# Kernel optimization log

Measured on AMD Instinct MI355X. Metric: run time of the kernel, lower is better.

The kernel has to match this reference:

```python
import jax, jax.numpy as jnp
import numpy as np

H = 1024   # hidden_size
I = 4096   # intermediate_size
E = 8      # num_local_experts
K = 2      # num_experts_per_tok
B, S = 2, 2048


def setup_inputs() -> dict:
    key = jax.random.key(0)
    ks = jax.random.split(key, 7)
    init = lambda k, shape, fan_in: (jax.random.normal(k, shape, jnp.float32)
                                     / np.float32(np.sqrt(fan_in)))
    return {
        "x": jax.random.normal(ks[0], (B, S, H), jnp.float32),
        "router_gate": init(ks[1], (E, H), H),   # router for gate_proj
        "w_gate": init(ks[2], (E, I, H), H),     # expert weights gate_proj
        "router_up": init(ks[3], (E, H), H),     # router for up_proj
        "w_up": init(ks[4], (E, I, H), H),       # expert weights up_proj
        "router_down": init(ks[5], (E, I), I),   # router for down_proj
        "w_down": init(ks[6], (E, H, I), I),     # expert weights down_proj
    }


def _moe_linear(x, router_w, expert_w):
    """Top-K routed linear. x:[T,din] router_w:[E,din] expert_w:[E,dout,din]."""
    n_exp = router_w.shape[0]
    logits = x @ router_w.T                      # [T, E]
    vals, idx = jax.lax.top_k(logits, K)         # [T, K]
    probs = jax.nn.softmax(vals, axis=-1)        # softmax over selected experts
    onehot = jax.nn.one_hot(idx, n_exp, dtype=x.dtype)    # [T, K, E]
    combine = jnp.einsum('tk,tke->te', probs, onehot)     # [T, E] sparse combine weights
    out = jnp.zeros((x.shape[0], expert_w.shape[1]), x.dtype)
    for e in range(n_exp):  # fixed small expert count
        out = out + combine[:, e:e + 1] * (x @ expert_w[e].T)
    return out


def reference(x, router_gate, w_gate, router_up, w_up, router_down, w_down):
    b, s, h = x.shape
    xt = x.reshape(b * s, h)                     # tokens [T, H]
    g = _moe_linear(xt, router_gate, w_gate)     # [T, I]
    u = _moe_linear(xt, router_up, w_up)         # [T, I]
    inter = jax.nn.silu(g) * u                   # SwiGLU
    d = _moe_linear(inter, router_down, w_down)  # [T, H]
    return d.reshape(b, s, h)
```

## Files before the change

### kernel.cpp

```cpp
#include <hip/hip_runtime.h>
#include <cmath>

typedef float    f32x4 __attribute__((ext_vector_type(4)));
typedef _Float16 f16x8 __attribute__((ext_vector_type(8)));
typedef _Float16 f16x4 __attribute__((ext_vector_type(4)));

#define T_NUM 4096
#define H_DIM 1024
#define I_DIM 4096
#define MAXTILES 40
#define GEMMBLK 768
#define CW3BLK 4096
#define CW1BLK 4096

#define M_COUNTS   0
#define M_CURSORS  48
#define M_OFFSETS  96
#define M_NTILES   144
#define M_TILE_E   152
#define M_TILE_M   392
#define M_TOPKI    1024
#define M_TOPKP    25600
#define M_STOK     50176
#define M_SPRB     74752

__device__ __forceinline__ float wave_sum(float v) {
  v += __shfl_xor(v, 32);
  v += __shfl_xor(v, 16);
  v += __shfl_xor(v, 8);
  v += __shfl_xor(v, 4);
  v += __shfl_xor(v, 2);
  v += __shfl_xor(v, 1);
  return v;
}

__device__ __forceinline__ void topk_write(int* meta, int layer, int t, const float* v) {
  int e0 = 0; float v0 = v[0];
  #pragma unroll
  for (int e = 1; e < 8; ++e) { if (v[e] > v0) { v0 = v[e]; e0 = e; } }
  int e1 = 0; float v1 = -3.4e38f;
  #pragma unroll
  for (int e = 0; e < 8; ++e) { if (e != e0 && v[e] > v1) { v1 = v[e]; e1 = e; } }
  float ex = expf(v1 - v0);
  float p0 = 1.f / (1.f + ex);
  float p1 = ex / (1.f + ex);
  meta[M_TOPKI + (layer * T_NUM + t) * 2    ] = e0;
  meta[M_TOPKI + (layer * T_NUM + t) * 2 + 1] = e1;
  ((float*)meta)[M_TOPKP + (layer * T_NUM + t) * 2    ] = p0;
  ((float*)meta)[M_TOPKP + (layer * T_NUM + t) * 2 + 1] = p1;
}

__global__ __launch_bounds__(256) void router_gu(const float* __restrict__ x,
    const float* __restrict__ Rg, const float* __restrict__ Ru, int* __restrict__ meta)
{
  int w = threadIdx.x >> 6, lane = threadIdx.x & 63;
  int t = blockIdx.x * 4 + w;
  const float* xr = x + (size_t)t * H_DIM + lane * 4;
  f32x4 xv[4];
  #pragma unroll
  for (int c = 0; c < 4; ++c) xv[c] = *(const f32x4*)(xr + c * 256);
  float lg[8], lu[8];
  #pragma unroll
  for (int e = 0; e < 8; ++e) {
    const float* rg = Rg + (size_t)e * H_DIM + lane * 4;
    const float* ru = Ru + (size_t)e * H_DIM + lane * 4;
    float sg = 0.f, su = 0.f;
    #pragma unroll
    for (int c = 0; c < 4; ++c) {
      f32x4 a = *(const f32x4*)(rg + c * 256);
      f32x4 b = *(const f32x4*)(ru + c * 256);
      sg += a[0]*xv[c][0] + a[1]*xv[c][1] + a[2]*xv[c][2] + a[3]*xv[c][3];
      su += b[0]*xv[c][0] + b[1]*xv[c][1] + b[2]*xv[c][2] + b[3]*xv[c][3];
    }
    lg[e] = wave_sum(sg);
    lu[e] = wave_sum(su);
  }
  if (lane == 0) {
    topk_write(meta, 0, t, lg);
    topk_write(meta, 1, t, lu);
  }
}

__global__ __launch_bounds__(256) void route_finalize(int* __restrict__ meta, int l0, int nl) {
  __shared__ int cnt_s[32];
  __shared__ int off_s[32];
  __shared__ int cur_s[32];
  int tid = threadIdx.x;
  if (tid < 32) { cnt_s[tid] = 0; cur_s[tid] = 0; }
  __syncthreads();
  for (int t = tid; t < T_NUM; t += 256) {
    for (int l = l0; l < l0 + nl; ++l) {
      int li = l - l0;
      #pragma unroll
      for (int k = 0; k < 2; ++k) {
        int e = meta[M_TOPKI + (l * T_NUM + t) * 2 + k];
        atomicAdd(&cnt_s[li * 16 + k * 8 + e], 1);
      }
    }
  }
  __syncthreads();
  if (tid == 0) {
    for (int l = l0; l < l0 + nl; ++l) {
      int li = l - l0;
      int off = 0;
      for (int k = 0; k < 2; ++k) {
        int nt = 0;
        for (int e = 0; e < 8; ++e) {
          int s = (l * 2 + k) * 8 + e;
          int c = cnt_s[li * 16 + k * 8 + e];
          meta[M_COUNTS + s] = c;
          meta[M_OFFSETS + s] = off;
          off_s[li * 16 + k * 8 + e] = off;
          for (int m = 0; m < c; m += 128) {
            meta[M_TILE_E + (l * 2 + k) * MAXTILES + nt] = e;
            meta[M_TILE_M + (l * 2 + k) * MAXTILES + nt] = m;
            ++nt;
          }
          off += c;
        }
        meta[M_NTILES + l * 2 + k] = nt;
      }
    }
  }
  __syncthreads();
  for (int t = tid; t < T_NUM; t += 256) {
    for (int l = l0; l < l0 + nl; ++l) {
      int li = l - l0;
      #pragma unroll
      for (int k = 0; k < 2; ++k) {
        int e = meta[M_TOPKI + (l * T_NUM + t) * 2 + k];
        float p = ((float*)meta)[M_TOPKP + (l * T_NUM + t) * 2 + k];
        int si = li * 16 + k * 8 + e;
        int pos = off_s[si] + atomicAdd(&cur_s[si], 1);
        meta[M_STOK + l * 8192 + pos] = t;
        ((float*)meta)[M_SPRB + l * 8192 + pos] = p;
      }
    }
  }
}

template<int SPLITS, int NB, int KT>
__device__ __forceinline__ void convert_lds_body(const float* __restrict__ W,
    _Float16* __restrict__ Whi, _Float16* __restrict__ Wlo, int blk,
    _Float16* sHi, _Float16* sLo)
{
  constexpr int KTG = KT / 2;
  constexpr int K   = KT * 32;
  int panel = blk / KTG;
  int ktg   = blk - panel * KTG;
  int t = threadIdx.x;
  int r = t >> 1, h = t & 1;

  const float* src = W + ((size_t)panel * 128 + r) * K + (ktg * 2 + h) * 32;
  f32x4 v[8];
  #pragma unroll
  for (int j = 0; j < 8; ++j) v[j] = *(const f32x4*)(src + j * 4);

  #pragma unroll
  for (int fq = 0; fq < 4; ++fq) {
    f16x8 hi8, lo8;
    #pragma unroll
    for (int q = 0; q < 8; ++q) {
      int idx = fq * 8 + q;
      float x = v[idx >> 2][idx & 3];
      _Float16 hx = (_Float16)x;
      hi8[q] = hx;
      if constexpr (SPLITS == 3) lo8[q] = (_Float16)(x - (float)hx);
    }
    int loff = h * 4096 + fq * 1024 + r * 8;
    *(f16x8*)(sHi + loff) = hi8;
    if constexpr (SPLITS == 3) *(f16x8*)(sLo + loff) = lo8;
  }
  __syncthreads();

  size_t base = ((size_t)panel * KT + ktg * 2) * 4096;
  #pragma unroll
  for (int j = 0; j < 4; ++j) {
    int o = (j * 256 + t) * 8;
    *(f16x8*)(Whi + base + o) = *(const f16x8*)(sHi + o);
  }
  if constexpr (SPLITS == 3) {
    #pragma unroll
    for (int j = 0; j < 4; ++j) {
      int o = (j * 256 + t) * 8;
      *(f16x8*)(Wlo + base + o) = *(const f16x8*)(sLo + o);
    }
  }
}

__device__ __forceinline__ void gather_a_body(const float* __restrict__ X,
    _Float16* __restrict__ Apass, const int* __restrict__ meta, int layer, int kk, int gb)
{
  int pass = layer * 2 + kk;
  int tile = gb >> 5;
  int kt   = gb & 31;
  if (tile >= meta[M_NTILES + pass]) return;
  int m0   = meta[M_TILE_M + pass * MAXTILES + tile];
  int e    = meta[M_TILE_E + pass * MAXTILES + tile];
  int sidx = pass * 8 + e;
  int cnt  = meta[M_COUNTS + sidx];
  int seg  = meta[M_OFFSETS + sidx];
  const int* stok = meta + M_STOK + layer * 8192 + seg;
  size_t cb = ((size_t)tile * 32 + kt) * 8192;
  #pragma unroll
  for (int j = 0; j < 2; ++j) {
    int idx = threadIdx.x * 2 + j;
    int fq = idx >> 7, row = idx & 127;
    int m = m0 + row; if (m >= cnt) m = cnt - 1;
    const float* src = X + (size_t)stok[m] * H_DIM + kt * 32 + fq * 8;
    f32x4 v0 = *(const f32x4*)src;
    f32x4 v1 = *(const f32x4*)(src + 4);
    f16x8 h, l;
    #pragma unroll
    for (int q = 0; q < 8; ++q) {
      float v = (q < 4) ? v0[q] : v1[q - 4];
      _Float16 hv = (_Float16)v;
      h[q] = hv;
      l[q] = (_Float16)(v - (float)hv);
    }
    *(f16x8*)(Apass + cb + (size_t)idx * 8) = h;
    *(f16x8*)(Apass + cb + 4096 + (size_t)idx * 8) = l;
  }
}

__device__ __forceinline__ void gather_d_body(const _Float16* __restrict__ Gi,
    _Float16* __restrict__ Ad, const int* __restrict__ meta, int kk, int gb)
{
  int pass = 4 + kk;
  int tile = gb >> 7;
  int kt   = gb & 127;
  if (tile >= meta[M_NTILES + pass]) return;
  int m0   = meta[M_TILE_M + pass * MAXTILES + tile];
  int e    = meta[M_TILE_E + pass * MAXTILES + tile];
  int sidx = pass * 8 + e;
  int cnt  = meta[M_COUNTS + sidx];
  int seg  = meta[M_OFFSETS + sidx];
  const int* stok = meta + M_STOK + 2 * 8192 + seg;
  size_t cb = ((size_t)tile * 128 + kt) * 4096;
  #pragma unroll
  for (int j = 0; j < 2; ++j) {
    int idx = threadIdx.x * 2 + j;
    int fq = idx >> 7, row = idx & 127;
    int m = m0 + row; if (m >= cnt) m = cnt - 1;
    f16x8 h = *(const f16x8*)(Gi + (size_t)stok[m] * I_DIM + kt * 32 + fq * 8);
    *(f16x8*)(Ad + cb + (size_t)idx * 8) = h;
  }
}

__global__ __launch_bounds__(256) void fused_cw3_ga(const float* __restrict__ W,
    _Float16* __restrict__ Whi, _Float16* __restrict__ Wlo,
    const float* __restrict__ X, _Float16* __restrict__ Atgt,
    const int* __restrict__ meta, int layer, int kk)
{
  __shared__ _Float16 sHi[8192];
  __shared__ _Float16 sLo[8192];
  int b = (int)blockIdx.x;
  if (b < CW3BLK) convert_lds_body<3, 32, 32>(W, Whi, Wlo, b, sHi, sLo);
  else gather_a_body(X, Atgt, meta, layer, kk, b - CW3BLK);
}

__global__ __launch_bounds__(256) void fused_cw3x2_ga(
    const float* __restrict__ Wg, _Float16* __restrict__ Wgh, _Float16* __restrict__ Wgl,
    const float* __restrict__ Wu, _Float16* __restrict__ Wuh, _Float16* __restrict__ Wul,
    const float* __restrict__ X, _Float16* __restrict__ Atgt, const int* __restrict__ meta)
{
  __shared__ _Float16 sHi[8192];
  __shared__ _Float16 sLo[8192];
  int b = (int)blockIdx.x;
  if (b < CW3BLK) convert_lds_body<3, 32, 32>(Wg, Wgh, Wgl, b, sHi, sLo);
  else if (b < 2 * CW3BLK) convert_lds_body<3, 32, 32>(Wu, Wuh, Wul, b - CW3BLK, sHi, sLo);
  else gather_a_body(X, Atgt, meta, 0, 0, b - 2 * CW3BLK);
}

__global__ __launch_bounds__(256) void fused_cw1_gd(const float* __restrict__ W,
    _Float16* __restrict__ Whi,
    const _Float16* __restrict__ Gi, _Float16* __restrict__ Adt,
    const int* __restrict__ meta, int kk)
{
  __shared__ _Float16 sHi[8192];
  int b = (int)blockIdx.x;
  if (b < CW1BLK) convert_lds_body<1, 8, 128>(W, Whi, Whi, b, sHi, sHi);
  else gather_d_body(Gi, Adt, meta, kk, b - CW1BLK);
}

__global__ __launch_bounds__(256) void gather_a_k(const float* __restrict__ X,
    _Float16* __restrict__ Apass, const int* __restrict__ meta, int layer, int kk)
{
  gather_a_body(X, Apass, meta, layer, kk, (int)blockIdx.x);
}

__device__ __forceinline__ void gload16(const _Float16* g, _Float16* l) {
  __builtin_amdgcn_global_load_lds(
      (const __attribute__((address_space(1))) void*)g,
      (__attribute__((address_space(3))) void*)l, 16, 0, 0);
}

template<int SPLITS, int ADD, int N, int NB, int STEPS, int SPLITK, int STEAL>
__global__ __launch_bounds__(256, 3) void moe_gemm9(
    const _Float16* __restrict__ Aimg,
    const _Float16* __restrict__ Whi, const _Float16* __restrict__ Wlo,
    float* __restrict__ Out, float* __restrict__ Scr,
    const int* __restrict__ meta, int layer, int kk,
    const void* __restrict__ aux_src, _Float16* __restrict__ aux_dst,
    int alayer, int akk)
{
  constexpr int NWG = MAXTILES * NB * SPLITK;
  constexpr int Q8  = NWG / 8;
  constexpr int WCH = (SPLITS == 3) ? 1 : 2;
  constexpr int NPER = GEMMBLK / 8;

  __shared__ __align__(16) _Float16 sA[3 * 8192];

  if constexpr (STEAL == 1) {
    for (int gb = (int)blockIdx.x; gb < MAXTILES * 32; gb += GEMMBLK)
      gather_a_body((const float*)aux_src, aux_dst, meta, alayer, akk, gb);
  } else if constexpr (STEAL == 2) {
    for (int gb = (int)blockIdx.x; gb < MAXTILES * 128; gb += GEMMBLK)
      gather_d_body((const _Float16*)aux_src, aux_dst, meta, akk, gb);
  }

  int xcd  = (int)blockIdx.x & 7;
  int slot = (int)blockIdx.x >> 3;
  int pass = layer * 2 + kk;
  int ntiles = meta[M_NTILES + pass];

  int tid = threadIdx.x, lane = tid & 63, w = tid >> 6;
  int wr = w >> 1, wc = w & 1, fr = lane & 15, fq = lane >> 4;
  int aoff = (fq * 128 + wr * 64 + fr) * 8;

  for (int base = slot; base < Q8; base += NPER) {
    int logical = xcd * Q8 + base;
    int kc = 0, rem = logical;
    if constexpr (SPLITK == 2) { kc = logical / (MAXTILES * NB); rem = logical - kc * (MAXTILES * NB); }
    int tx = rem / NB;
    int ny = rem - tx * NB;
    if (tx >= ntiles) continue;

    int e    = meta[M_TILE_E + pass * MAXTILES + tx];
    int m0   = meta[M_TILE_M + pass * MAXTILES + tx];
    int sidx = pass * 8 + e;
    int cnt  = meta[M_COUNTS + sidx];
    int seg  = meta[M_OFFSETS + sidx];
    int n0   = ny * 128;

    const int*   stok = meta + M_STOK + layer * 8192 + seg;
    const float* sprb = (const float*)meta + M_SPRB + layer * 8192 + seg;

    const _Float16* At = Aimg + ((size_t)tx * SPLITK + kc) * STEPS * 8192;
    size_t wpanel = (size_t)(e * NB + ny) * (STEPS * WCH * SPLITK) * 4096;
    int kb = kc * STEPS * WCH;
    const _Float16* WhL = Whi + wpanel + (size_t)kb * 4096 + (fq * 128 + wc * 64 + fr) * 8;
    const _Float16* WlL = Wlo + wpanel + (size_t)kb * 4096 + (fq * 128 + wc * 64 + fr) * 8;

    auto stageA = [&](int it, int slot2) {
      const _Float16* s0 = At + (size_t)it * 8192 + w * 1024 + lane * 8;
      _Float16* d0 = sA + slot2 * 8192 + w * 1024;
      gload16(s0,        d0);
      gload16(s0 + 512,  d0 + 512);
      gload16(s0 + 4096, d0 + 4096);
      gload16(s0 + 4608, d0 + 4608);
    };
    auto loadW = [&](int it, f16x8 (&wh)[WCH][4], f16x8 (&wl)[1][4]) {
      #pragma unroll
      for (int c = 0; c < WCH; ++c) {
        size_t cb = (size_t)(it * WCH + c) * 4096;
        #pragma unroll
        for (int ni = 0; ni < 4; ++ni) wh[c][ni] = *(const f16x8*)(WhL + cb + ni * 128);
      }
      if constexpr (SPLITS == 3) {
        size_t cb = (size_t)it * 4096;
        #pragma unroll
        for (int ni = 0; ni < 4; ++ni) wl[0][ni] = *(const f16x8*)(WlL + cb + ni * 128);
      }
    };

    f32x4 acc[4][4];
    #pragma unroll
    for (int i = 0; i < 4; ++i)
      #pragma unroll
      for (int j = 0; j < 4; ++j) acc[i][j] = f32x4{0.f, 0.f, 0.f, 0.f};

    f16x8 w0h[WCH][4], w0l[1][4], w1h[WCH][4], w1l[1][4];
    int rc = 0, rs = 2;

    auto step = [&](int it, f16x8 (&cwh)[WCH][4], f16x8 (&cwl)[1][4],
                    f16x8 (&nwh)[WCH][4], f16x8 (&nwl)[1][4]) {
      int it2 = (it + 2 < STEPS) ? it + 2 : STEPS - 1;
      int it1 = (it + 1 < STEPS) ? it + 1 : STEPS - 1;
      stageA(it2, rs);
      loadW(it1, nwh, nwl);
      __builtin_amdgcn_sched_barrier(0);

      const _Float16* A0 = sA + rc * 8192;
      __builtin_amdgcn_s_setprio(1);
      if constexpr (SPLITS == 3) {
        f16x8 ah[4], al[4];
        #pragma unroll
        for (int mi = 0; mi < 4; ++mi) ah[mi] = *(const f16x8*)(A0 + aoff + mi * 128);
        #pragma unroll
        for (int mi = 0; mi < 4; ++mi) al[mi] = *(const f16x8*)(A0 + 4096 + aoff + mi * 128);
        #pragma unroll
        for (int mi = 0; mi < 4; ++mi)
          #pragma unroll
          for (int ni = 0; ni < 4; ++ni)
            acc[mi][ni] = __builtin_amdgcn_mfma_f32_16x16x32_f16(ah[mi], cwh[0][ni], acc[mi][ni], 0, 0, 0);
        #pragma unroll
        for (int mi = 0; mi < 4; ++mi)
          #pragma unroll
          for (int ni = 0; ni < 4; ++ni)
            acc[mi][ni] = __builtin_amdgcn_mfma_f32_16x16x32_f16(ah[mi], cwl[0][ni], acc[mi][ni], 0, 0, 0);
        #pragma unroll
        for (int mi = 0; mi < 4; ++mi)
          #pragma unroll
          for (int ni = 0; ni < 4; ++ni)
            acc[mi][ni] = __builtin_amdgcn_mfma_f32_16x16x32_f16(al[mi], cwh[0][ni], acc[mi][ni], 0, 0, 0);
      } else {
        #pragma unroll
        for (int c = 0; c < WCH; ++c) {
          f16x8 ah[4];
          #pragma unroll
          for (int mi = 0; mi < 4; ++mi) ah[mi] = *(const f16x8*)(A0 + c * 4096 + aoff + mi * 128);
          #pragma unroll
          for (int mi = 0; mi < 4; ++mi)
            #pragma unroll
            for (int ni = 0; ni < 4; ++ni)
              acc[mi][ni] = __builtin_amdgcn_mfma_f32_16x16x32_f16(ah[mi], cwh[c][ni], acc[mi][ni], 0, 0, 0);
        }
      }
      __builtin_amdgcn_s_setprio(0);

      __builtin_amdgcn_sched_barrier(0);
      asm volatile("s_waitcnt vmcnt(12)" ::: "memory");
      __builtin_amdgcn_s_barrier();
      __builtin_amdgcn_sched_barrier(0);
      rc = (rc == 2) ? 0 : rc + 1;
      rs = (rs == 2) ? 0 : rs + 1;
    };

    asm volatile("s_waitcnt vmcnt(0)" ::: "memory");
    __builtin_amdgcn_s_barrier();
    stageA(0, 0);
    stageA(1 < STEPS ? 1 : 0, 1);
    loadW(0, w0h, w0l);
    __builtin_amdgcn_sched_barrier(0);
    asm volatile("s_waitcnt vmcnt(12)" ::: "memory");
    __builtin_amdgcn_s_barrier();
    __builtin_amdgcn_sched_barrier(0);

    for (int it = 0; it < STEPS; it += 2) {
      step(it,     w0h, w0l, w1h, w1l);
      step(it + 1, w1h, w1l, w0h, w0l);
    }

    float* dst = (SPLITK == 2 && kc == 1) ? Scr : Out;
    #pragma unroll
    for (int mi = 0; mi < 4; ++mi) {
      #pragma unroll
      for (int jj = 0; jj < 4; ++jj) {
        int lm = wr * 64 + mi * 16 + fq * 4 + jj;
        int gm = m0 + lm;
        if (gm < cnt) {
          int tok = stok[gm];
          float p = sprb[gm];
          float* orow = dst + (size_t)tok * N + n0 + wc * 64 + fr;
          #pragma unroll
          for (int ni = 0; ni < 4; ++ni) {
            float v = p * acc[mi][ni][jj];
            if constexpr (ADD) orow[ni * 16] += v; else orow[ni * 16] = v;
          }
        }
      }
    }
  }
}

__global__ __launch_bounds__(256) void swiglu_router(const float* __restrict__ g,
    const float* __restrict__ u, const float* __restrict__ Rd,
    _Float16* __restrict__ gi, int* __restrict__ meta)
{
  int t = blockIdx.x, tid = threadIdx.x;
  float part[8];
  #pragma unroll
  for (int e = 0; e < 8; ++e) part[e] = 0.f;
  const float* gr = g + (size_t)t * I_DIM;
  const float* ur = u + (size_t)t * I_DIM;
  _Float16*    ir = gi + (size_t)t * I_DIM;
  #pragma unroll
  for (int cc = 0; cc < 4; ++cc) {
    int i = cc * 1024 + tid * 4;
    f32x4 gv = *(const f32x4*)(gr + i);
    f32x4 uv = *(const f32x4*)(ur + i);
    f32x4 iv;
    f16x4 hv;
    #pragma unroll
    for (int j = 0; j < 4; ++j) {
      float xx = gv[j];
      iv[j] = (xx / (1.f + expf(-xx))) * uv[j];
      hv[j] = (_Float16)iv[j];
    }
    *(f16x4*)(ir + i) = hv;
    #pragma unroll
    for (int e = 0; e < 8; ++e) {
      f32x4 rv = *(const f32x4*)(Rd + (size_t)e * I_DIM + i);
      part[e] += rv[0]*iv[0] + rv[1]*iv[1] + rv[2]*iv[2] + rv[3]*iv[3];
    }
  }
  __shared__ float red[4][8];
  int w = tid >> 6, lane = tid & 63;
  #pragma unroll
  for (int e = 0; e < 8; ++e) {
    float s = wave_sum(part[e]);
    if (lane == 0) red[w][e] = s;
  }
  __syncthreads();
  if (tid == 0) {
    float lg[8];
    #pragma unroll
    for (int e = 0; e < 8; ++e) lg[e] = red[0][e] + red[1][e] + red[2][e] + red[3][e];
    topk_write(meta, 2, t, lg);
  }
}

__global__ __launch_bounds__(256) void combine_kernel(float* __restrict__ out,
                                                      const float* __restrict__ scr)
{
  int i = blockIdx.x * 1024 + threadIdx.x * 4;
  f32x4 a = *(const f32x4*)(out + i);
  f32x4 b = *(const f32x4*)(scr + i);
  #pragma unroll
  for (int j = 0; j < 4; ++j) a[j] += b[j];
  *(f32x4*)(out + i) = a;
}

extern "C" void kernel_launch(void* const* d_in, const int* in_sizes, int n_in,
                              void* d_out, int out_size, void* d_ws, size_t ws_size,
                              hipStream_t stream)
{
  const float* x  = (const float*)d_in[0];
  const float* Rg = (const float*)d_in[1];
  const float* Wg = (const float*)d_in[2];
  const float* Ru = (const float*)d_in[3];
  const float* Wu = (const float*)d_in[4];
  const float* Rd = (const float*)d_in[5];
  const float* Wd = (const float*)d_in[6];
  float* out = (float*)d_out;
  char* ws = (char*)d_ws;

  const size_t MB64 = 67108864;
  const size_t A_SZ = 20971520;

  if (ws_size >= (size_t)445644800) {
    _Float16* Wgh = (_Float16*)ws;
    _Float16* Wgl = (_Float16*)(ws + MB64);
    _Float16* Wuh = (_Float16*)(ws + 2 * MB64);
    _Float16* Wul = (_Float16*)(ws + 3 * MB64);
    float* g = (float*)(ws + 4 * MB64);
    float* u = (float*)(ws + 5 * MB64);
    int* meta = (int*)(ws + 6 * MB64);
    _Float16* A0 = (_Float16*)(ws + 6 * MB64 + 1048576);
    _Float16* A2 = (_Float16*)(ws + 6 * MB64 + 1048576 + A_SZ);
    _Float16* A1  = (_Float16*)u;
    _Float16* gi  = (_Float16*)Wgl;
    _Float16* Wdh = Wgh;
    _Float16* Ad0 = (_Float16*)u;
    _Float16* Ad1 = (_Float16*)g;
    float* dscr   = (float*)A0;

    router_gu<<<dim3(T_NUM / 4), 256, 0, stream>>>(x, Rg, Ru, meta);
    route_finalize<<<dim3(1), 256, 0, stream>>>(meta, 0, 2);

    fused_cw3x2_ga<<<dim3(2 * CW3BLK + MAXTILES * 32), 256, 0, stream>>>(
        Wg, Wgh, Wgl, Wu, Wuh, Wul, x, A0, meta);
    moe_gemm9<3, 0, I_DIM, 32, 32, 1, 1><<<dim3(GEMMBLK), 256, 0, stream>>>(
        A0, Wgh, Wgl, g, g, meta, 0, 0, x, A1, 0, 1);
    moe_gemm9<3, 1, I_DIM, 32, 32, 1, 1><<<dim3(GEMMBLK), 256, 0, stream>>>(
        A1, Wgh, Wgl, g, g, meta, 0, 1, x, A0, 1, 0);
    moe_gemm9<3, 0, I_DIM, 32, 32, 1, 1><<<dim3(GEMMBLK), 256, 0, stream>>>(
        A0, Wuh, Wul, u, u, meta, 1, 0, x, A2, 1, 1);
    moe_gemm9<3, 1, I_DIM, 32, 32, 1, 0><<<dim3(GEMMBLK), 256, 0, stream>>>(
        A2, Wuh, Wul, u, u, meta, 1, 1, x, A2, 0, 0);

    swiglu_router<<<dim3(T_NUM), 256, 0, stream>>>(g, u, Rd, gi, meta);
    route_finalize<<<dim3(1), 256, 0, stream>>>(meta, 2, 1);

    fused_cw1_gd<<<dim3(CW1BLK + MAXTILES * 128), 256, 0, stream>>>(Wd, Wdh, gi, Ad0, meta, 0);
    moe_gemm9<1, 0, H_DIM, 8, 32, 2, 2><<<dim3(GEMMBLK), 256, 0, stream>>>(
        Ad0, Wdh, Wdh, out, dscr, meta, 2, 0, gi, Ad1, 0, 1);
    moe_gemm9<1, 1, H_DIM, 8, 32, 2, 0><<<dim3(GEMMBLK), 256, 0, stream>>>(
        Ad1, Wdh, Wdh, out, dscr, meta, 2, 1, gi, Ad1, 0, 1);
    combine_kernel<<<dim3(T_NUM), 256, 0, stream>>>(out, dscr);
  } else {
    _Float16* Wth = (_Float16*)ws;
    _Float16* Wtl = (_Float16*)(ws + MB64);
    float* g   = (float*)(ws + (size_t)134217728);
    float* u   = (float*)(ws + (size_t)201326592);
    int*  meta = (int*)(ws + (size_t)268435456);
    _Float16* A0 = (_Float16*)(ws + (size_t)269484032);
    _Float16* A1 = (_Float16*)u;
    _Float16* gi = (_Float16*)Wtl;
    _Float16* Ad0 = (_Float16*)u;
    _Float16* Ad1 = (_Float16*)g;
    float* dscr = (float*)A0;

    router_gu<<<dim3(T_NUM / 4), 256, 0, stream>>>(x, Rg, Ru, meta);
    route_finalize<<<dim3(1), 256, 0, stream>>>(meta, 0, 2);

    fused_cw3_ga<<<dim3(CW3BLK + MAXTILES * 32), 256, 0, stream>>>(Wg, Wth, Wtl, x, A0, meta, 0, 0);
    moe_gemm9<3, 0, I_DIM, 32, 32, 1, 1><<<dim3(GEMMBLK), 256, 0, stream>>>(
        A0, Wth, Wtl, g, g, meta, 0, 0, x, A1, 0, 1);
    moe_gemm9<3, 1, I_DIM, 32, 32, 1, 1><<<dim3(GEMMBLK), 256, 0, stream>>>(
        A1, Wth, Wtl, g, g, meta, 0, 1, x, A0, 1, 0);
    fused_cw3_ga<<<dim3(CW3BLK), 256, 0, stream>>>(Wu, Wth, Wtl, x, A0, meta, 0, 0);
    moe_gemm9<3, 0, I_DIM, 32, 32, 1, 0><<<dim3(GEMMBLK), 256, 0, stream>>>(
        A0, Wth, Wtl, u, u, meta, 1, 0, x, A0, 0, 0);
    gather_a_k<<<dim3(MAXTILES * 32), 256, 0, stream>>>(x, A0, meta, 1, 1);
    moe_gemm9<3, 1, I_DIM, 32, 32, 1, 0><<<dim3(GEMMBLK), 256, 0, stream>>>(
        A0, Wth, Wtl, u, u, meta, 1, 1, x, A0, 0, 0);

    swiglu_router<<<dim3(T_NUM), 256, 0, stream>>>(g, u, Rd, gi, meta);
    route_finalize<<<dim3(1), 256, 0, stream>>>(meta, 2, 1);

    fused_cw1_gd<<<dim3(CW1BLK + MAXTILES * 128), 256, 0, stream>>>(Wd, Wth, gi, Ad0, meta, 0);
    moe_gemm9<1, 0, H_DIM, 8, 32, 2, 2><<<dim3(GEMMBLK), 256, 0, stream>>>(
        Ad0, Wth, Wth, out, dscr, meta, 2, 0, gi, Ad1, 0, 1);
    moe_gemm9<1, 1, H_DIM, 8, 32, 2, 0><<<dim3(GEMMBLK), 256, 0, stream>>>(
        Ad1, Wth, Wth, out, dscr, meta, 2, 1, gi, Ad1, 0, 1);
    combine_kernel<<<dim3(T_NUM), 256, 0, stream>>>(out, dscr);
  }
}
```

Baseline: 935.7 us.

## Merge down-projection top-k passes into one GEMM with four-way split buffers

The down projection used to run two GEMM passes, one per top-k slot, with a split-K scratch buffer and an accumulate into the output. It now gathers both passes' activations in one fused convert/gather launch and runs a single GEMM kernel covering both passes and both K halves. Each pass/K-half pair writes to its own float buffer, and a four-input combine kernel sums them. This removes a launch and the read-modify-write accumulation and gives a larger, better-balanced grid. The cost is extra workspace traffic: four full-size float buffers are written and then read back.

```diff
diff --git a/kernel.cpp b/kernel.cpp
--- a/kernel.cpp
+++ b/kernel.cpp
@@ -12,6 +12,7 @@
 #define GEMMBLK 768
 #define CW3BLK 4096
 #define CW1BLK 4096
+#define GDBLK  5120
 
 #define M_COUNTS   0
 #define M_CURSORS  48
@@ -274,13 +275,14 @@
 
 __global__ __launch_bounds__(256) void fused_cw1_gd(const float* __restrict__ W,
     _Float16* __restrict__ Whi,
-    const _Float16* __restrict__ Gi, _Float16* __restrict__ Adt,
-    const int* __restrict__ meta, int kk)
+    const _Float16* __restrict__ Gi, _Float16* __restrict__ Adt0,
+    _Float16* __restrict__ Adt1, const int* __restrict__ meta)
 {
   __shared__ _Float16 sHi[8192];
   int b = (int)blockIdx.x;
   if (b < CW1BLK) convert_lds_body<1, 8, 128>(W, Whi, Whi, b, sHi, sHi);
-  else gather_d_body(Gi, Adt, meta, kk, b - CW1BLK);
+  else if (b < CW1BLK + GDBLK) gather_d_body(Gi, Adt0, meta, 0, b - CW1BLK);
+  else gather_d_body(Gi, Adt1, meta, 1, b - CW1BLK - GDBLK);
 }
 
 __global__ __launch_bounds__(256) void gather_a_k(const float* __restrict__ X,
@@ -474,6 +476,142 @@
   }
 }
 
+__global__ __launch_bounds__(256, 3) void moe_gemm_dn(
+    const _Float16* __restrict__ Ad0, const _Float16* __restrict__ Ad1,
+    const _Float16* __restrict__ Whi,
+    float* __restrict__ Db, const int* __restrict__ meta)
+{
+  constexpr int NB = 8, STEPS = 32, WCH = 2;
+  constexpr int NWG = MAXTILES * NB * 2;
+  constexpr int Q16 = (2 * NWG) / 8;
+  constexpr int NPER = GEMMBLK / 8;
+
+  __shared__ __align__(16) _Float16 sA[3 * 8192];
+
+  int xcd  = (int)blockIdx.x & 7;
+  int slot = (int)blockIdx.x >> 3;
+
+  int tid = threadIdx.x, lane = tid & 63, w = tid >> 6;
+  int wr = w >> 1, wc = w & 1, fr = lane & 15, fq = lane >> 4;
+  int aoff = (fq * 128 + wr * 64 + fr) * 8;
+
+  for (int base = slot; base < Q16; base += NPER) {
+    int logical = xcd * Q16 + base;
+    int kkp  = logical / NWG;
+    int rem  = logical - kkp * NWG;
+    int kc   = rem / (MAXTILES * NB);
+    int rem2 = rem - kc * (MAXTILES * NB);
+    int tx = rem2 / NB;
+    int ny = rem2 - tx * NB;
+    int pass = 4 + kkp;
+    if (tx >= meta[M_NTILES + pass]) continue;
+
+    int e    = meta[M_TILE_E + pass * MAXTILES + tx];
+    int m0   = meta[M_TILE_M + pass * MAXTILES + tx];
+    int sidx = pass * 8 + e;
+    int cnt  = meta[M_COUNTS + sidx];
+    int seg  = meta[M_OFFSETS + sidx];
+    int n0   = ny * 128;
+
+    const int*   stok = meta + M_STOK + 2 * 8192 + seg;
+    const float* sprb = (const float*)meta + M_SPRB + 2 * 8192 + seg;
+
+    const _Float16* Aimg = kkp ? Ad1 : Ad0;
+    const _Float16* At = Aimg + ((size_t)tx * 2 + kc) * STEPS * 8192;
+    size_t wpanel = (size_t)(e * NB + ny) * (STEPS * WCH * 2) * 4096;
+    int kb = kc * STEPS * WCH;
+    const _Float16* WhL = Whi + wpanel + (size_t)kb * 4096 + (fq * 128 + wc * 64 + fr) * 8;
+
+    auto stageA = [&](int it, int slot2) {
+      const _Float16* s0 = At + (size_t)it * 8192 + w * 1024 + lane * 8;
+      _Float16* d0 = sA + slot2 * 8192 + w * 1024;
+      gload16(s0,        d0);
+      gload16(s0 + 512,  d0 + 512);
+      gload16(s0 + 4096, d0 + 4096);
+      gload16(s0 + 4608, d0 + 4608);
+    };
+    auto loadW = [&](int it, f16x8 (&wh)[WCH][4]) {
+      #pragma unroll
+      for (int c = 0; c < WCH; ++c) {
+        size_t cb = (size_t)(it * WCH + c) * 4096;
+        #pragma unroll
+        for (int ni = 0; ni < 4; ++ni) wh[c][ni] = *(const f16x8*)(WhL + cb + ni * 128);
+      }
+    };
+
+    f32x4 acc[4][4];
+    #pragma unroll
+    for (int i = 0; i < 4; ++i)
+      #pragma unroll
+      for (int j = 0; j < 4; ++j) acc[i][j] = f32x4{0.f, 0.f, 0.f, 0.f};
+
+    f16x8 w0h[WCH][4], w1h[WCH][4];
+    int rc = 0, rs = 2;
+
+    auto step = [&](int it, f16x8 (&cwh)[WCH][4], f16x8 (&nwh)[WCH][4]) {
+      int it2 = (it + 2 < STEPS) ? it + 2 : STEPS - 1;
+      int it1 = (it + 1 < STEPS) ? it + 1 : STEPS - 1;
+      stageA(it2, rs);
+      loadW(it1, nwh);
+      __builtin_amdgcn_sched_barrier(0);
+
+      const _Float16* A0 = sA + rc * 8192;
+      __builtin_amdgcn_s_setprio(1);
+      #pragma unroll
+      for (int c = 0; c < WCH; ++c) {
+        f16x8 ah[4];
+        #pragma unroll
+        for (int mi = 0; mi < 4; ++mi) ah[mi] = *(const f16x8*)(A0 + c * 4096 + aoff + mi * 128);
+        #pragma unroll
+        for (int mi = 0; mi < 4; ++mi)
+          #pragma unroll
+          for (int ni = 0; ni < 4; ++ni)
+            acc[mi][ni] = __builtin_amdgcn_mfma_f32_16x16x32_f16(ah[mi], cwh[c][ni], acc[mi][ni], 0, 0, 0);
+      }
+      __builtin_amdgcn_s_setprio(0);
+
+      __builtin_amdgcn_sched_barrier(0);
+      asm volatile("s_waitcnt vmcnt(12)" ::: "memory");
+      __builtin_amdgcn_s_barrier();
+      __builtin_amdgcn_sched_barrier(0);
+      rc = (rc == 2) ? 0 : rc + 1;
+      rs = (rs == 2) ? 0 : rs + 1;
+    };
+
+    asm volatile("s_waitcnt vmcnt(0)" ::: "memory");
+    __builtin_amdgcn_s_barrier();
+    stageA(0, 0);
+    stageA(1, 1);
+    loadW(0, w0h);
+    __builtin_amdgcn_sched_barrier(0);
+    asm volatile("s_waitcnt vmcnt(12)" ::: "memory");
+    __builtin_amdgcn_s_barrier();
+    __builtin_amdgcn_sched_barrier(0);
+
+    for (int it = 0; it < STEPS; it += 2) {
+      step(it,     w0h, w1h);
+      step(it + 1, w1h, w0h);
+    }
+
+    float* dst = Db + (size_t)(kkp * 2 + kc) * T_NUM * H_DIM;
+    #pragma unroll
+    for (int mi = 0; mi < 4; ++mi) {
+      #pragma unroll
+      for (int jj = 0; jj < 4; ++jj) {
+        int lm = wr * 64 + mi * 16 + fq * 4 + jj;
+        int gm = m0 + lm;
+        if (gm < cnt) {
+          int tok = stok[gm];
+          float p = sprb[gm];
+          float* orow = dst + (size_t)tok * H_DIM + n0 + wc * 64 + fr;
+          #pragma unroll
+          for (int ni = 0; ni < 4; ++ni) orow[ni * 16] = p * acc[mi][ni][jj];
+        }
+      }
+    }
+  }
+}
+
 __global__ __launch_bounds__(256) void swiglu_router(const float* __restrict__ g,
     const float* __restrict__ u, const float* __restrict__ Rd,
     _Float16* __restrict__ gi, int* __restrict__ meta)
@@ -529,6 +667,20 @@
   f32x4 b = *(const f32x4*)(scr + i);
   #pragma unroll
   for (int j = 0; j < 4; ++j) a[j] += b[j];
+  *(f32x4*)(out + i) = a;
+}
+
+__global__ __launch_bounds__(256) void combine4_kernel(float* __restrict__ out,
+                                                       const float* __restrict__ db)
+{
+  const size_t S = (size_t)T_NUM * H_DIM;
+  int i = blockIdx.x * 1024 + threadIdx.x * 4;
+  f32x4 a = *(const f32x4*)(db + i);
+  f32x4 b = *(const f32x4*)(db + S + i);
+  f32x4 c = *(const f32x4*)(db + 2 * S + i);
+  f32x4 d = *(const f32x4*)(db + 3 * S + i);
+  #pragma unroll
+  for (int j = 0; j < 4; ++j) a[j] = (a[j] + b[j]) + (c[j] + d[j]);
   *(f32x4*)(out + i) = a;
 }
 
@@ -564,7 +716,7 @@
     _Float16* Wdh = Wgh;
     _Float16* Ad0 = (_Float16*)u;
     _Float16* Ad1 = (_Float16*)g;
-    float* dscr   = (float*)A0;
+    float* db     = (float*)(ws + 2 * MB64);
 
     router_gu<<<dim3(T_NUM / 4), 256, 0, stream>>>(x, Rg, Ru, meta);
     route_finalize<<<dim3(1), 256, 0, stream>>>(meta, 0, 2);
@@ -583,12 +735,9 @@
     swiglu_router<<<dim3(T_NUM), 256, 0, stream>>>(g, u, Rd, gi, meta);
     route_finalize<<<dim3(1), 256, 0, stream>>>(meta, 2, 1);
 
-    fused_cw1_gd<<<dim3(CW1BLK + MAXTILES * 128), 256, 0, stream>>>(Wd, Wdh, gi, Ad0, meta, 0);
-    moe_gemm9<1, 0, H_DIM, 8, 32, 2, 2><<<dim3(GEMMBLK), 256, 0, stream>>>(
-        Ad0, Wdh, Wdh, out, dscr, meta, 2, 0, gi, Ad1, 0, 1);
-    moe_gemm9<1, 1, H_DIM, 8, 32, 2, 0><<<dim3(GEMMBLK), 256, 0, stream>>>(
-        Ad1, Wdh, Wdh, out, dscr, meta, 2, 1, gi, Ad1, 0, 1);
-    combine_kernel<<<dim3(T_NUM), 256, 0, stream>>>(out, dscr);
+    fused_cw1_gd<<<dim3(CW1BLK + 2 * GDBLK), 256, 0, stream>>>(Wd, Wdh, gi, Ad0, Ad1, meta);
+    moe_gemm_dn<<<dim3(GEMMBLK), 256, 0, stream>>>(Ad0, Ad1, Wdh, db, meta);
+    combine4_kernel<<<dim3(T_NUM), 256, 0, stream>>>(out, db);
   } else {
     _Float16* Wth = (_Float16*)ws;
     _Float16* Wtl = (_Float16*)(ws + MB64);
@@ -620,7 +769,7 @@
     swiglu_router<<<dim3(T_NUM), 256, 0, stream>>>(g, u, Rd, gi, meta);
     route_finalize<<<dim3(1), 256, 0, stream>>>(meta, 2, 1);
 
-    fused_cw1_gd<<<dim3(CW1BLK + MAXTILES * 128), 256, 0, stream>>>(Wd, Wth, gi, Ad0, meta, 0);
+    fused_cw1_gd<<<dim3(CW1BLK + GDBLK), 256, 0, stream>>>(Wd, Wth, gi, Ad0, Ad1, meta);
     moe_gemm9<1, 0, H_DIM, 8, 32, 2, 2><<<dim3(GEMMBLK), 256, 0, stream>>>(
         Ad0, Wth, Wth, out, dscr, meta, 2, 0, gi, Ad1, 0, 1);
     moe_gemm9<1, 1, H_DIM, 8, 32, 2, 0><<<dim3(GEMMBLK), 256, 0, stream>>>(
```

Measured after the change: 926.3 us. Within noise of the previous version (-1.0%).
